# Optimization experiments

Hardware: AMD Instinct MI355X
Metric: run time of the kernel (lower is better)

The kernel has to match this reference:

```python
import jax, jax.numpy as jnp
import numpy as np

B, S, D = 1, 2048, 2048
NH, NKV, HD = 16, 8, 128
FF = 8192
L = 2
V = 32000
THETA = 10000.0
EPS = 1e-5
SCALE = 0.02


def setup_inputs() -> dict:
    key = jax.random.key(0)
    ks = jax.random.split(key, 16)
    return {
        "input_ids": jax.random.randint(ks[0], (B, S), 0, V, dtype=jnp.int32),
        "embed": jax.random.normal(ks[1], (V, D), jnp.float32) * SCALE,
        "Wq": jax.random.normal(ks[2], (L, D, NH * HD), jnp.float32) * SCALE,
        "Wk": jax.random.normal(ks[3], (L, D, NKV * HD), jnp.float32) * SCALE,
        "Wv": jax.random.normal(ks[4], (L, D, NKV * HD), jnp.float32) * SCALE,
        "Wo": jax.random.normal(ks[5], (L, NH * HD, D), jnp.float32) * SCALE,
        "Wgate": jax.random.normal(ks[6], (L, D, FF), jnp.float32) * SCALE,
        "Wup": jax.random.normal(ks[7], (L, D, FF), jnp.float32) * SCALE,
        "Wdown": jax.random.normal(ks[8], (L, FF, D), jnp.float32) * SCALE,
        "norm_attn": jnp.ones((L, D), jnp.float32),
        "norm_mlp": jnp.ones((L, D), jnp.float32),
        "norm_final": jnp.ones((D,), jnp.float32),
        "lm_head": jax.random.normal(ks[9], (D, V), jnp.float32) * SCALE,
        "D1": jax.random.normal(ks[10], (S,), jnp.float32) + 2.0,
        "D2": jax.random.normal(ks[11], (HD,), jnp.float32) + 2.0,
        "D3": jax.random.normal(ks[12], (S,), jnp.float32) + 2.0,
    }


def _rms_norm(x, w):
    return x * jax.lax.rsqrt(jnp.mean(x * x, axis=-1, keepdims=True) + EPS) * w


def _rotate_half(x):
    x1, x2 = jnp.split(x, 2, axis=-1)
    return jnp.concatenate([-x2, x1], axis=-1)


def _forward(input_ids, embed, Wq, Wk, Wv, Wo, Wgate, Wup, Wdown,
             norm_attn, norm_mlp, norm_final, lm_head, D1, D2, D3):
    # RoPE tables: [1,1,S,HD]
    inv_freq = 1.0 / (THETA ** (jnp.arange(0, HD, 2, dtype=jnp.float32) / HD))
    freqs = jnp.arange(S, dtype=jnp.float32)[:, None] * inv_freq[None, :]
    emb = jnp.concatenate([freqs, freqs], axis=-1)
    cos = jnp.cos(emb)[None, None]
    sin = jnp.sin(emb)[None, None]
    causal = jnp.tril(jnp.ones((S, S), dtype=bool))
    neg = jnp.finfo(jnp.float32).min
    D1i, D2i, D3i = 1.0 / D1, 1.0 / D2, 1.0 / D3
    n_rep = NH // NKV

    h = embed[input_ids]  # [B,S,D]
    for l in range(L):
        # --- attention block ---
        x = _rms_norm(h, norm_attn[l])
        q = (x @ Wq[l]).reshape(B, S, NH, HD).transpose(0, 2, 1, 3)   # [B,NH,S,HD]
        k = (x @ Wk[l]).reshape(B, S, NKV, HD).transpose(0, 2, 1, 3)  # [B,NKV,S,HD]
        v = (x @ Wv[l]).reshape(B, S, NKV, HD).transpose(0, 2, 1, 3)
        q = q * cos + _rotate_half(q) * sin
        k = k * cos + _rotate_half(k) * sin
        # repeat_kv (GQA)
        k = jnp.repeat(k, n_rep, axis=1)
        v = jnp.repeat(v, n_rep, axis=1)
        # TEE diagonal encryption: Q' = D1 Q D2, K'^T = D2^-1 K^T D3
        q_enc = q * D1[None, None, :, None] * D2[None, None, None, :]
        k_enc = k * D3[None, None, :, None] * D2i[None, None, None, :]
        scores = jnp.einsum('bhqd,bhkd->bhqk', q_enc, k_enc)
        # decrypt: D1^-1 (Q'K'^T) D3^-1  (mathematically cancels encryption)
        scores = scores * D1i[None, None, :, None] * D3i[None, None, None, :]
        scores = scores / jnp.sqrt(jnp.float32(HD))
        scores = jnp.where(causal[None, None], scores, neg)
        probs = jax.nn.softmax(scores, axis=-1)
        o = jnp.einsum('bhqk,bhkd->bhqd', probs, v)
        o = o.transpose(0, 2, 1, 3).reshape(B, S, NH * HD)
        h = h + o @ Wo[l]
        # --- SwiGLU MLP block ---
        x = _rms_norm(h, norm_mlp[l])
        h = h + (jax.nn.silu(x @ Wgate[l]) * (x @ Wup[l])) @ Wdown[l]

    h = _rms_norm(h, norm_final)
    return h @ lm_head  # logits [B,S,V]


def reference(input_ids, embed, Wq, Wk, Wv, Wo, Wgate, Wup, Wdown,
              norm_attn, norm_mlp, norm_final, lm_head, D1, D2, D3):
    return _forward(input_ids, embed, Wq, Wk, Wv, Wo, Wgate, Wup, Wdown,
                    norm_attn, norm_mlp, norm_final, lm_head, D1, D2, D3)
```

## Files before the change

### kernel.cpp

```cpp
#include <hip/hip_runtime.h>
#include <cstdint>
#include <cstddef>

typedef __attribute__((ext_vector_type(4))) float f32x4;
typedef __attribute__((ext_vector_type(8))) short short8;
typedef __attribute__((ext_vector_type(4))) unsigned int u32x4;

static const int TS = 2048;
static const int DM = 2048;
static const int NHEAD = 16, NKVH = 8, HDIM = 128;
static const int FFD = 8192;
static const int NVOC = 32000;
static const int QKVN = 4096;

__device__ __forceinline__ unsigned short f2bf(float f){
  unsigned int u = __builtin_bit_cast(unsigned int, f);
  u += 0x7FFFu + ((u >> 16) & 1u);
  return (unsigned short)(u >> 16);
}
__device__ __forceinline__ float bf2f(short h){
  unsigned int u = ((unsigned int)(unsigned short)h) << 16;
  return __builtin_bit_cast(float, u);
}
__device__ __forceinline__ f32x4 mfma16(short8 a, short8 b, f32x4 c){
  return __builtin_amdgcn_mfma_f32_16x16x32_bf16(a, b, c, 0, 0, 0);
}
__device__ __forceinline__ void gload16(const void* g, void* l){
  __builtin_amdgcn_global_load_lds(
      (const __attribute__((address_space(1))) unsigned int*)g,
      (__attribute__((address_space(3))) unsigned int*)l, 16, 0, 0);
}

__global__ void rope_tables_k(float* __restrict__ cosT, float* __restrict__ sinT){
  int idx = blockIdx.x * 256 + threadIdx.x;
  int s = idx >> 6, j = idx & 63;
  float inv = exp2f(-(float)j * (13.287712379549449f / 64.0f));
  float ang = (float)s * inv;
  cosT[idx] = cosf(ang);
  sinT[idx] = sinf(ang);
}

__global__ void embed_k(const int* __restrict__ ids, const float* __restrict__ E,
                        float* __restrict__ h){
  int s = blockIdx.x, tid = threadIdx.x;
  long id = ids[s];
  const f32x4* src = (const f32x4*)(E + id * (long)DM);
  f32x4* dst = (f32x4*)(h + (long)s * DM);
  dst[tid] = src[tid];
  dst[tid + 256] = src[tid + 256];
}

__global__ void rmsnorm_k(const float* __restrict__ x, const float* __restrict__ w,
                          short* __restrict__ out){
  int s = blockIdx.x, tid = threadIdx.x;
  const float* row = x + (long)s * DM;
  f32x4 v0 = *(const f32x4*)&row[tid * 8];
  f32x4 v1 = *(const f32x4*)&row[tid * 8 + 4];
  float ss = v0[0]*v0[0] + v0[1]*v0[1] + v0[2]*v0[2] + v0[3]*v0[3]
           + v1[0]*v1[0] + v1[1]*v1[1] + v1[2]*v1[2] + v1[3]*v1[3];
  #pragma unroll
  for (int off = 32; off; off >>= 1) ss += __shfl_xor(ss, off);
  __shared__ float sred[4];
  int wave = tid >> 6, lane = tid & 63;
  if (lane == 0) sred[wave] = ss;
  __syncthreads();
  float tot = sred[0] + sred[1] + sred[2] + sred[3];
  float r = rsqrtf(tot * (1.0f / (float)DM) + 1e-5f);
  f32x4 w0 = *(const f32x4*)&w[tid * 8];
  f32x4 w1 = *(const f32x4*)&w[tid * 8 + 4];
  short8 o;
  #pragma unroll
  for (int j = 0; j < 4; j++) o[j] = (short)f2bf(v0[j] * r * w0[j]);
  #pragma unroll
  for (int j = 0; j < 4; j++) o[4 + j] = (short)f2bf(v1[j] * r * w1[j]);
  *(short8*)&out[(long)s * DM + tid * 8] = o;
}

__global__ void transpose_k(const float* __restrict__ B, short* __restrict__ Bt,
                            int K, int N){
  __shared__ float t[64][65];
  int tid = threadIdx.x;
  int kb = blockIdx.y * 64, nb = blockIdx.x * 64;
  int r0 = tid >> 4, c4 = tid & 15;
  #pragma unroll
  for (int p = 0; p < 4; p++){
    int r = r0 + p * 16;
    f32x4 v = *(const f32x4*)&B[(long)(kb + r) * N + nb + c4 * 4];
    t[r][c4*4+0] = v[0]; t[r][c4*4+1] = v[1]; t[r][c4*4+2] = v[2]; t[r][c4*4+3] = v[3];
  }
  __syncthreads();
  int n0 = tid >> 3, k0 = (tid & 7) * 8;
  #pragma unroll
  for (int p = 0; p < 2; p++){
    int n = n0 + p * 32;
    short8 o;
    #pragma unroll
    for (int j = 0; j < 8; j++) o[j] = (short)f2bf(t[k0 + j][n]);
    *(short8*)&Bt[(long)(nb + n) * K + kb + k0] = o;
  }
}

__global__ void vtrans_k(const short* __restrict__ vb, short* __restrict__ vtb, int stride){
  int s0 = blockIdx.x * 64, kv = blockIdx.y;
  int tid = threadIdx.x;
  int s = s0 + (tid & 63);
  int d0 = (tid >> 6) * 8;
  #pragma unroll
  for (int p = 0; p < 4; p++){
    int d = d0 + p * 32;
    short8 v = *(const short8*)&vb[(long)s * stride + kv * HDIM + d];
    #pragma unroll
    for (int j = 0; j < 8; j++)
      vtb[(long)(kv * HDIM + d + j) * TS + s] = v[j];
  }
}

__global__ void rope_apply_k(short* __restrict__ buf, const float* __restrict__ cosT,
                             const float* __restrict__ sinT, int nh, int stride, int coloff){
  int idx = blockIdx.x * 256 + threadIdx.x;
  int j = idx & 63;
  int t = idx >> 6;
  int hh = t % nh;
  int s = t / nh;
  long base = (long)s * stride + coloff + hh * HDIM + j;
  float c = cosT[s * 64 + j], sn = sinT[s * 64 + j];
  float x1 = bf2f(buf[base]), x2 = bf2f(buf[base + 64]);
  buf[base]      = (short)f2bf(x1 * c - x2 * sn);
  buf[base + 64] = (short)f2bf(x2 * c + x1 * sn);
}

__global__ void reduce4_k(const float* __restrict__ p, float* __restrict__ h){
  const long stride = (long)TS * DM;
  long i = ((long)blockIdx.x * 256 + threadIdx.x) * 4;
  f32x4 a = *(const f32x4*)&h[i];
  f32x4 v0 = *(const f32x4*)&p[i];
  f32x4 v1 = *(const f32x4*)&p[i + stride];
  f32x4 v2 = *(const f32x4*)&p[i + 2 * stride];
  f32x4 v3 = *(const f32x4*)&p[i + 3 * stride];
  a = a + ((v0 + v1) + (v2 + v3));
  *(f32x4*)&h[i] = a;
}

template<int EPI>
__global__ __launch_bounds__(512, 2)
void gemm256(const short* __restrict__ A, int lda,
             const short* __restrict__ Bt, int ldb,
             float* __restrict__ Cf, short* __restrict__ Cb,
             const short* __restrict__ Xtra, int N, int K){
  __shared__ short lds[2][2][16384];
  const int tid = threadIdx.x;
  const int wid = tid >> 6, lane = tid & 63;
  const int wr = wid >> 2, wc = wid & 3;
  const int fr = lane & 15, fch = lane >> 4;
  const int nt = K >> 6;
  const int nIter = nt >> 1;

  const int z = blockIdx.y;
  A  += (long)z * K;
  Bt += (long)z * K;

  const int nbt = N >> 8;
  const int nwg = nbt << 3;
  const int q = nwg >> 3;
  const int swz = (blockIdx.x & 7) * q + (blockIdx.x >> 3);
  const int mb = swz & 7, nb = swz >> 3;

  const short* Abase = A  + (long)(mb * 256 + fr) * lda + fch * 8;
  const short* Bbase = Bt + (long)(nb * 256 + fr) * ldb + fch * 8;
  const int gA = ((wid >> 2) << 3) | (wid & 3);
  const int gB = ((wid >> 1) << 2) | (wid & 1);

  short8 a[4][2], b[2][2];
  f32x4 acc[8][4] = {};

#define STAGE_A(buf, beta, tau) do{ \
    const int g_ = gA | ((beta) << 2); \
    const short* gp_ = Abase + (long)(g_ * 16) * lda + (long)(tau) * 64; \
    gload16(gp_,      &lds[buf][0][(g_ * 2 + 0) * 512]); \
    gload16(gp_ + 32, &lds[buf][0][(g_ * 2 + 1) * 512]); \
  }while(0)
#define STAGE_B(buf, beta, tau) do{ \
    const int g_ = gB | ((beta) << 1); \
    const short* gp_ = Bbase + (long)(g_ * 16) * ldb + (long)(tau) * 64; \
    gload16(gp_,      &lds[buf][1][(g_ * 2 + 0) * 512]); \
    gload16(gp_ + 32, &lds[buf][1][(g_ * 2 + 1) * 512]); \
  }while(0)
#define LDA(buf, mh) do{ \
    _Pragma("unroll") \
    for (int j_ = 0; j_ < 4; j_++){ \
      const int o_ = (wr * 8 + (mh) * 4 + j_) * 1024 + fch * 128 + fr * 8; \
      a[j_][0] = *(const short8*)&lds[buf][0][o_]; \
      a[j_][1] = *(const short8*)&lds[buf][0][o_ + 512]; \
    } }while(0)
#define LDB(buf, nh) do{ \
    _Pragma("unroll") \
    for (int j_ = 0; j_ < 2; j_++){ \
      const int o_ = (wc * 4 + (nh) * 2 + j_) * 1024 + fch * 128 + fr * 8; \
      b[j_][0] = *(const short8*)&lds[buf][1][o_]; \
      b[j_][1] = *(const short8*)&lds[buf][1][o_ + 512]; \
    } }while(0)
#define SYNC_MF(mh, nh) do{ \
    __builtin_amdgcn_s_barrier(); \
    asm volatile("s_waitcnt lgkmcnt(0)" ::: "memory"); \
    __builtin_amdgcn_s_setprio(1); \
    _Pragma("unroll") \
    for (int j_ = 0; j_ < 4; j_++) \
      _Pragma("unroll") \
      for (int i_ = 0; i_ < 2; i_++){ \
        acc[(mh)*4+j_][(nh)*2+i_] = mfma16(a[j_][0], b[i_][0], acc[(mh)*4+j_][(nh)*2+i_]); \
        acc[(mh)*4+j_][(nh)*2+i_] = mfma16(a[j_][1], b[i_][1], acc[(mh)*4+j_][(nh)*2+i_]); \
      } \
    __builtin_amdgcn_s_setprio(0); \
    __builtin_amdgcn_s_barrier(); \
  }while(0)

  STAGE_A(0, 0, 0); STAGE_B(0, 0, 0); STAGE_B(0, 1, 0); STAGE_A(0, 1, 0);
  STAGE_A(1, 0, 1); STAGE_B(1, 1, 1); STAGE_A(1, 1, 1);
  asm volatile("s_waitcnt vmcnt(6)" ::: "memory");
  __builtin_amdgcn_s_barrier();

  for (int it = 0; it < nIter; ++it){
    const int t = it * 2;
    const int t2 = (t + 2 < nt) ? t + 2 : nt - 1;
    const int t3 = (t + 3 < nt) ? t + 3 : nt - 1;
    LDA(0, 0); LDB(0, 0); STAGE_B(1, 0, t + 1);
    SYNC_MF(0, 0);
    LDB(0, 1); STAGE_A(0, 0, t2);
    SYNC_MF(0, 1);
    LDA(0, 1); STAGE_B(0, 1, t2);
    SYNC_MF(1, 1);
    LDB(0, 0); STAGE_A(0, 1, t2);
    asm volatile("s_waitcnt vmcnt(6)" ::: "memory");
    SYNC_MF(1, 0);
    LDA(1, 0); LDB(1, 0); STAGE_B(0, 0, t2);
    SYNC_MF(0, 0);
    LDB(1, 1); STAGE_A(1, 0, t3);
    SYNC_MF(0, 1);
    LDA(1, 1); STAGE_B(1, 1, t3);
    SYNC_MF(1, 1);
    LDB(1, 0); STAGE_A(1, 1, t3);
    asm volatile("s_waitcnt vmcnt(6)" ::: "memory");
    SYNC_MF(1, 0);
  }
  asm volatile("s_waitcnt vmcnt(0)" ::: "memory");

#undef STAGE_A
#undef STAGE_B
#undef LDA
#undef LDB
#undef SYNC_MF

  const int rb0 = mb * 256 + wr * 128 + fch * 4;
  const int cb0 = nb * 256 + wc * 64 + fr;
  const long pbase = (EPI == 5) ? (long)z * ((long)TS * N) : 0;
  #pragma unroll
  for (int m = 0; m < 8; m++)
    #pragma unroll
    for (int n = 0; n < 4; n++)
      #pragma unroll
      for (int i = 0; i < 4; i++){
        long idx = (long)(rb0 + m * 16 + i) * N + (cb0 + n * 16);
        float v = acc[m][n][i];
        if constexpr (EPI == 0) Cf[idx] = v;
        else if constexpr (EPI == 1) Cb[idx] = (short)f2bf(v);
        else if constexpr (EPI == 3){
          float sg = 1.0f / (1.0f + __expf(-v));
          Cb[idx] = (short)f2bf(v * sg);
        } else if constexpr (EPI == 4){
          float g = bf2f(Xtra[idx]);
          Cb[idx] = (short)f2bf(g * v);
        } else {
          Cf[pbase + idx] = v;
        }
      }
}

template<int EPI>
__global__ __launch_bounds__(256)
void gemm_bt(const short* __restrict__ A, const short* __restrict__ Bt,
             float* __restrict__ Cf, short* __restrict__ Cb,
             const short* __restrict__ Xtra, int N, int K){
  __shared__ short As[4096];
  __shared__ short Bs[4096];
  const int tid = threadIdx.x;
  const int wave = tid >> 6, lane = tid & 63;
  const int wr = wave >> 1, wc = wave & 1;
  const int mb = blockIdx.y, nb = blockIdx.x;

  const int srow = lane & 15;
  const int scol = (lane >> 4) * 8;
  const short* ApL0 = A + (long)(mb * 128 + wave * 16 + srow) * K + scol;
  const short* ApL1 = ApL0 + (long)64 * K;
  const short* BpL0 = Bt + (long)(nb * 128 + wave * 16 + srow) * K + scol;
  const short* BpL1 = BpL0 + (long)64 * K;

  f32x4 acc[4][4] = {};
  const int fr = lane & 15, fch = lane >> 4;

  for (int kb = 0; kb < K; kb += 32){
    __syncthreads();
    gload16(ApL0 + kb, &As[wave * 512]);
    gload16(ApL1 + kb, &As[(4 + wave) * 512]);
    gload16(BpL0 + kb, &Bs[wave * 512]);
    gload16(BpL1 + kb, &Bs[(4 + wave) * 512]);
    __syncthreads();
    short8 a[4], b[4];
    #pragma unroll
    for (int m = 0; m < 4; m++)
      a[m] = *(const short8*)&As[(wr * 4 + m) * 512 + fch * 128 + fr * 8];
    #pragma unroll
    for (int n = 0; n < 4; n++)
      b[n] = *(const short8*)&Bs[(wc * 4 + n) * 512 + fch * 128 + fr * 8];
    #pragma unroll
    for (int m = 0; m < 4; m++)
      #pragma unroll
      for (int n = 0; n < 4; n++)
        acc[m][n] = mfma16(a[m], b[n], acc[m][n]);
  }

  const int rb = mb * 128 + wr * 64 + (lane >> 4) * 4;
  const int cb = nb * 128 + wc * 64 + (lane & 15);
  #pragma unroll
  for (int m = 0; m < 4; m++)
    #pragma unroll
    for (int n = 0; n < 4; n++)
      #pragma unroll
      for (int i = 0; i < 4; i++){
        long idx = (long)(rb + m * 16 + i) * N + (cb + n * 16);
        float v = acc[m][n][i];
        if constexpr (EPI == 0) Cf[idx] = v;
        else if constexpr (EPI == 1) Cb[idx] = (short)f2bf(v);
        else if constexpr (EPI == 2) Cf[idx] += v;
        else if constexpr (EPI == 3){
          float sg = 1.0f / (1.0f + __expf(-v));
          Cb[idx] = (short)f2bf(v * sg);
        } else {
          float g = bf2f(Xtra[idx]);
          Cb[idx] = (short)f2bf(g * v);
        }
      }
}

__device__ __forceinline__ int qoff(int r, int cB){ return r * 256 + (cB ^ ((r & 7) << 4)); }
__device__ __forceinline__ int voff(int d, int cB){ return d * 128 + (cB ^ ((d & 7) << 4)); }
__device__ __forceinline__ int poff(int r, int cB){ return r * 128 + (cB ^ ((r & 7) << 4)); }

__global__ __launch_bounds__(256)
void attn_k(const short* __restrict__ qb, const short* __restrict__ kb,
            const short* __restrict__ vtb, short* __restrict__ ob){
  __shared__ short Qs[64 * 128];
  __shared__ short Ks[64 * 128];
  __shared__ short Vt[128 * 64];
  __shared__ short Ps[64 * 64];
  const int tid = threadIdx.x, wave = tid >> 6, lane = tid & 63;
  const int qt = blockIdx.x, head = blockIdx.y, kvh = head >> 1;
  const float scale = 0.08838834764831845f;

  {
    int r0 = tid >> 4, c16 = tid & 15;
    #pragma unroll
    for (int p = 0; p < 4; p++){
      int r = r0 + p * 16;
      u32x4 v = *(const u32x4*)&qb[(long)(qt * 64 + r) * QKVN + head * HDIM + c16 * 8];
      *(u32x4*)((char*)Qs + qoff(r, c16 * 16)) = v;
    }
  }

  float mrun[4] = {-1e30f, -1e30f, -1e30f, -1e30f};
  float lrun[4] = {0.f, 0.f, 0.f, 0.f};
  f32x4 accO[8] = {};

  for (int kt = 0; kt <= qt; kt++){
    __syncthreads();
    {
      int r0 = tid >> 4, c16 = tid & 15;
      #pragma unroll
      for (int p = 0; p < 4; p++){
        int r = r0 + p * 16;
        u32x4 v = *(const u32x4*)&kb[(long)(kt * 64 + r) * QKVN + kvh * HDIM + c16 * 8];
        *(u32x4*)((char*)Ks + qoff(r, c16 * 16)) = v;
      }
      int vr0 = tid >> 3, vc = tid & 7;
      #pragma unroll
      for (int p = 0; p < 4; p++){
        int d = vr0 + p * 32;
        u32x4 v = *(const u32x4*)&vtb[(long)(kvh * HDIM + d) * TS + kt * 64 + vc * 8];
        *(u32x4*)((char*)Vt + voff(d, vc * 16)) = v;
      }
    }
    __syncthreads();

    f32x4 sacc[4] = {};
    #pragma unroll
    for (int k4 = 0; k4 < 4; k4++){
      short8 aq = *(const short8*)((const char*)Qs +
                   qoff(wave * 16 + (lane & 15), k4 * 64 + (lane >> 4) * 16));
      #pragma unroll
      for (int n = 0; n < 4; n++){
        short8 bk = *(const short8*)((const char*)Ks +
                     qoff(n * 16 + (lane & 15), k4 * 64 + (lane >> 4) * 16));
        sacc[n] = mfma16(aq, bk, sacc[n]);
      }
    }

    const bool diag = (kt == qt);
    float mt[4] = {-1e30f, -1e30f, -1e30f, -1e30f};
    #pragma unroll
    for (int n = 0; n < 4; n++)
      #pragma unroll
      for (int i = 0; i < 4; i++){
        float v = sacc[n][i] * scale;
        if (diag){
          int rr = (lane >> 4) * 4 + i + wave * 16;
          int cc = n * 16 + (lane & 15);
          if (cc > rr) v = -1e30f;
        }
        sacc[n][i] = v;
        mt[i] = fmaxf(mt[i], v);
      }
    #pragma unroll
    for (int off = 1; off < 16; off <<= 1)
      #pragma unroll
      for (int i = 0; i < 4; i++) mt[i] = fmaxf(mt[i], __shfl_xor(mt[i], off));
    float alpha[4], rsum[4];
    #pragma unroll
    for (int i = 0; i < 4; i++){
      float mn = fmaxf(mrun[i], mt[i]);
      alpha[i] = __expf(mrun[i] - mn);
      mrun[i] = mn;
      rsum[i] = 0.f;
    }
    #pragma unroll
    for (int n = 0; n < 4; n++)
      #pragma unroll
      for (int i = 0; i < 4; i++){
        float p = __expf(sacc[n][i] - mrun[i]);
        sacc[n][i] = p;
        rsum[i] += p;
      }
    #pragma unroll
    for (int off = 1; off < 16; off <<= 1)
      #pragma unroll
      for (int i = 0; i < 4; i++) rsum[i] += __shfl_xor(rsum[i], off);
    #pragma unroll
    for (int i = 0; i < 4; i++) lrun[i] = lrun[i] * alpha[i] + rsum[i];

    #pragma unroll
    for (int n = 0; n < 4; n++)
      #pragma unroll
      for (int i = 0; i < 4; i++){
        int rr = wave * 16 + (lane >> 4) * 4 + i;
        int cc = n * 16 + (lane & 15);
        *(short*)((char*)Ps + poff(rr, cc * 2)) = (short)f2bf(sacc[n][i]);
      }

    #pragma unroll
    for (int n = 0; n < 8; n++)
      #pragma unroll
      for (int i = 0; i < 4; i++) accO[n][i] *= alpha[i];
    #pragma unroll
    for (int ks = 0; ks < 2; ks++){
      short8 ap = *(const short8*)((const char*)Ps +
                   poff(wave * 16 + (lane & 15), ks * 64 + (lane >> 4) * 16));
      #pragma unroll
      for (int n = 0; n < 8; n++){
        short8 bv = *(const short8*)((const char*)Vt +
                     voff(n * 16 + (lane & 15), ks * 64 + (lane >> 4) * 16));
        accO[n] = mfma16(ap, bv, accO[n]);
      }
    }
  }

  #pragma unroll
  for (int i = 0; i < 4; i++){
    float inv = 1.0f / lrun[i];
    int rr = qt * 64 + wave * 16 + (lane >> 4) * 4 + i;
    #pragma unroll
    for (int n = 0; n < 8; n++){
      int cc = head * HDIM + n * 16 + (lane & 15);
      ob[(long)rr * DM + cc] = (short)f2bf(accO[n][i] * inv);
    }
  }
}

extern "C" void kernel_launch(void* const* d_in, const int* in_sizes, int n_in,
                              void* d_out, int out_size, void* d_ws, size_t ws_size,
                              hipStream_t stream){
  (void)in_sizes; (void)n_in; (void)out_size; (void)ws_size;
  const int*   ids = (const int*)d_in[0];
  const float* E   = (const float*)d_in[1];
  const float* Wq  = (const float*)d_in[2];
  const float* Wk  = (const float*)d_in[3];
  const float* Wv  = (const float*)d_in[4];
  const float* Wo  = (const float*)d_in[5];
  const float* Wg  = (const float*)d_in[6];
  const float* Wu  = (const float*)d_in[7];
  const float* Wd  = (const float*)d_in[8];
  const float* nA  = (const float*)d_in[9];
  const float* nM  = (const float*)d_in[10];
  const float* nF  = (const float*)d_in[11];
  const float* LMH = (const float*)d_in[12];
  float* out = (float*)d_out;

  char* ws = (char*)d_ws;
  size_t off = 0;
  auto alloc = [&](size_t bytes){ void* p = ws + off; off += (bytes + 255) & ~(size_t)255; return p; };
  float* h    = (float*)alloc((size_t)TS * DM * 4);
  short* xb   = (short*)alloc((size_t)TS * DM * 2);
  short* qkvb = (short*)alloc((size_t)TS * QKVN * 2);
  short* vtb  = (short*)alloc((size_t)NKVH * HDIM * TS * 2);
  short* obuf = (short*)alloc((size_t)TS * DM * 2);
  short* sg   = (short*)alloc((size_t)TS * FFD * 2);
  short* actb = (short*)alloc((size_t)TS * FFD * 2);
  float* cosT = (float*)alloc((size_t)TS * 64 * 4);
  float* sinT = (float*)alloc((size_t)TS * 64 * 4);
  short* wT   = (short*)alloc((size_t)NVOC * DM * 2);
  float* pPart = (float*)((char*)wT + (size_t)36 * 1024 * 1024);

  rope_tables_k<<<512, 256, 0, stream>>>(cosT, sinT);
  embed_k<<<TS, 256, 0, stream>>>(ids, E, h);

  for (int l = 0; l < 2; l++){
    rmsnorm_k<<<TS, 256, 0, stream>>>(h, nA + (size_t)l * DM, xb);
    transpose_k<<<dim3(32, 32), 256, 0, stream>>>(Wq + (size_t)l * DM * DM, wT, DM, DM);
    transpose_k<<<dim3(16, 32), 256, 0, stream>>>(Wk + (size_t)l * DM * 1024, wT + (size_t)2048 * DM, DM, 1024);
    transpose_k<<<dim3(16, 32), 256, 0, stream>>>(Wv + (size_t)l * DM * 1024, wT + (size_t)3072 * DM, DM, 1024);
    gemm256<1><<<dim3(128), 512, 0, stream>>>(xb, DM, wT, DM, nullptr, qkvb, nullptr, QKVN, DM);
    rope_apply_k<<<8192, 256, 0, stream>>>(qkvb, cosT, sinT, NHEAD, QKVN, 0);
    rope_apply_k<<<4096, 256, 0, stream>>>(qkvb, cosT, sinT, NKVH, QKVN, 2048);
    vtrans_k<<<dim3(32, 8), 256, 0, stream>>>(qkvb + 3072, vtb, QKVN);
    attn_k<<<dim3(32, 16), 256, 0, stream>>>(qkvb, qkvb + 2048, vtb, obuf);
    transpose_k<<<dim3(32, 32), 256, 0, stream>>>(Wo + (size_t)l * DM * DM, wT, DM, DM);
    gemm_bt<2><<<dim3(16, 16), 256, 0, stream>>>(obuf, wT, h, nullptr, nullptr, DM, DM);
    rmsnorm_k<<<TS, 256, 0, stream>>>(h, nM + (size_t)l * DM, xb);
    transpose_k<<<dim3(128, 32), 256, 0, stream>>>(Wg + (size_t)l * DM * FFD, wT, DM, FFD);
    gemm256<3><<<dim3(256), 512, 0, stream>>>(xb, DM, wT, DM, nullptr, sg, nullptr, FFD, DM);
    transpose_k<<<dim3(128, 32), 256, 0, stream>>>(Wu + (size_t)l * DM * FFD, wT, DM, FFD);
    gemm256<4><<<dim3(256), 512, 0, stream>>>(xb, DM, wT, DM, nullptr, actb, sg, FFD, DM);
    transpose_k<<<dim3(32, 128), 256, 0, stream>>>(Wd + (size_t)l * FFD * DM, wT, FFD, DM);
    gemm256<5><<<dim3(64, 4), 512, 0, stream>>>(actb, FFD, wT, FFD, pPart, nullptr, nullptr, DM, FFD / 4);
    reduce4_k<<<4096, 256, 0, stream>>>(pPart, h);
  }

  rmsnorm_k<<<TS, 256, 0, stream>>>(h, nF, xb);
  transpose_k<<<dim3(500, 32), 256, 0, stream>>>(LMH, wT, DM, NVOC);
  gemm256<0><<<dim3(1000), 512, 0, stream>>>(xb, DM, wT, DM, out, nullptr, nullptr, NVOC, DM);
}
```

Baseline: 1.543 ms.

## Restructure GEMM mainloop to 4-buffer K=32 pipeline with register ping-pong

Rewrites the gemm256 main loop so each K step is 32 wide instead of 64, and rotates four LDS buffers instead of two. Fragments are held in even/odd register sets so the next tile's LDS reads overlap the current MFMAs. This cuts barriers per MFMA group, from two per 8-MFMA block to two per tile, and uses sched_barrier to keep loads interleaved with compute. The risks are a deeper prefetch with tighter vmcnt accounting and shorter K tiles, which mean more iterations and more loop overhead. The final vmcnt(0) drain was also removed.

```diff
diff --git a/kernel.cpp b/kernel.cpp
--- a/kernel.cpp
+++ b/kernel.cpp
@@ -147,13 +147,12 @@
              const short* __restrict__ Bt, int ldb,
              float* __restrict__ Cf, short* __restrict__ Cb,
              const short* __restrict__ Xtra, int N, int K){
-  __shared__ short lds[2][2][16384];
+  __shared__ short lds[4][2][8192];
   const int tid = threadIdx.x;
   const int wid = tid >> 6, lane = tid & 63;
   const int wr = wid >> 2, wc = wid & 3;
   const int fr = lane & 15, fch = lane >> 4;
-  const int nt = K >> 6;
-  const int nIter = nt >> 1;
+  const int nt = K >> 5;
 
   const int z = blockIdx.y;
   A  += (long)z * K;
@@ -167,88 +166,69 @@
 
   const short* Abase = A  + (long)(mb * 256 + fr) * lda + fch * 8;
   const short* Bbase = Bt + (long)(nb * 256 + fr) * ldb + fch * 8;
-  const int gA = ((wid >> 2) << 3) | (wid & 3);
-  const int gB = ((wid >> 1) << 2) | (wid & 1);
-
-  short8 a[4][2], b[2][2];
+  const int gA0 = wid * 2, gA1 = wid * 2 + 1;
+
+  short8 aE[4], aO[4], bE[2], bO[2];
   f32x4 acc[8][4] = {};
 
-#define STAGE_A(buf, beta, tau) do{ \
-    const int g_ = gA | ((beta) << 2); \
-    const short* gp_ = Abase + (long)(g_ * 16) * lda + (long)(tau) * 64; \
-    gload16(gp_,      &lds[buf][0][(g_ * 2 + 0) * 512]); \
-    gload16(gp_ + 32, &lds[buf][0][(g_ * 2 + 1) * 512]); \
+#define STG_A(bufc, g_, tau_) \
+  gload16(Abase + (long)((g_) * 16) * lda + (long)(tau_) * 32, &lds[bufc][0][(g_) * 512])
+#define STG_B(bufc, g_, tau_) \
+  gload16(Bbase + (long)((g_) * 16) * ldb + (long)(tau_) * 32, &lds[bufc][1][(g_) * 512])
+#define RDA(dst, bufc, mh) do{ \
+    _Pragma("unroll") \
+    for (int j_ = 0; j_ < 4; j_++) \
+      dst[j_] = *(const short8*)&lds[bufc][0][(wr * 8 + (mh) * 4 + j_) * 512 + fch * 128 + fr * 8]; \
   }while(0)
-#define STAGE_B(buf, beta, tau) do{ \
-    const int g_ = gB | ((beta) << 1); \
-    const short* gp_ = Bbase + (long)(g_ * 16) * ldb + (long)(tau) * 64; \
-    gload16(gp_,      &lds[buf][1][(g_ * 2 + 0) * 512]); \
-    gload16(gp_ + 32, &lds[buf][1][(g_ * 2 + 1) * 512]); \
+#define RDB(dst, bufc, nh) do{ \
+    _Pragma("unroll") \
+    for (int i_ = 0; i_ < 2; i_++) \
+      dst[i_] = *(const short8*)&lds[bufc][1][(wc * 4 + (nh) * 2 + i_) * 512 + fch * 128 + fr * 8]; \
   }while(0)
-#define LDA(buf, mh) do{ \
-    _Pragma("unroll") \
-    for (int j_ = 0; j_ < 4; j_++){ \
-      const int o_ = (wr * 8 + (mh) * 4 + j_) * 1024 + fch * 128 + fr * 8; \
-      a[j_][0] = *(const short8*)&lds[buf][0][o_]; \
-      a[j_][1] = *(const short8*)&lds[buf][0][o_ + 512]; \
-    } }while(0)
-#define LDB(buf, nh) do{ \
-    _Pragma("unroll") \
-    for (int j_ = 0; j_ < 2; j_++){ \
-      const int o_ = (wc * 4 + (nh) * 2 + j_) * 1024 + fch * 128 + fr * 8; \
-      b[j_][0] = *(const short8*)&lds[buf][1][o_]; \
-      b[j_][1] = *(const short8*)&lds[buf][1][o_ + 512]; \
-    } }while(0)
-#define SYNC_MF(mh, nh) do{ \
-    __builtin_amdgcn_s_barrier(); \
-    asm volatile("s_waitcnt lgkmcnt(0)" ::: "memory"); \
+#define MM8(va, vb, mh, nh) do{ \
     __builtin_amdgcn_s_setprio(1); \
     _Pragma("unroll") \
     for (int j_ = 0; j_ < 4; j_++) \
       _Pragma("unroll") \
-      for (int i_ = 0; i_ < 2; i_++){ \
-        acc[(mh)*4+j_][(nh)*2+i_] = mfma16(a[j_][0], b[i_][0], acc[(mh)*4+j_][(nh)*2+i_]); \
-        acc[(mh)*4+j_][(nh)*2+i_] = mfma16(a[j_][1], b[i_][1], acc[(mh)*4+j_][(nh)*2+i_]); \
-      } \
+      for (int i_ = 0; i_ < 2; i_++) \
+        acc[(mh)*4+j_][(nh)*2+i_] = mfma16(va[j_], vb[i_], acc[(mh)*4+j_][(nh)*2+i_]); \
     __builtin_amdgcn_s_setprio(0); \
+  }while(0)
+#define SB __builtin_amdgcn_sched_barrier(0)
+
+#define TILE(t_, bufR, bufN, bufS, bC, bNx) do{ \
+    const int tau_ = ((t_) + 2 < nt) ? (t_) + 2 : nt - 1; \
+    RDB(bNx, bufR, 1); STG_A(bufS, gA0, tau_); SB; MM8(aE, bC, 0, 0); \
+    RDA(aO,  bufR, 1); STG_A(bufS, gA1, tau_); SB; MM8(aE, bNx, 0, 1); \
+    asm volatile("s_waitcnt vmcnt(2)" ::: "memory"); \
+    __builtin_amdgcn_s_barrier(); \
+    RDA(aE,  bufN, 0); STG_B(bufS, gA0, tau_); SB; MM8(aO, bNx, 1, 1); \
+    RDB(bNx, bufN, 0); STG_B(bufS, gA1, tau_); SB; MM8(aO, bC, 1, 0); \
     __builtin_amdgcn_s_barrier(); \
   }while(0)
 
-  STAGE_A(0, 0, 0); STAGE_B(0, 0, 0); STAGE_B(0, 1, 0); STAGE_A(0, 1, 0);
-  STAGE_A(1, 0, 1); STAGE_B(1, 1, 1); STAGE_A(1, 1, 1);
-  asm volatile("s_waitcnt vmcnt(6)" ::: "memory");
+  STG_A(0, gA0, 0); STG_A(0, gA1, 0); STG_B(0, gA0, 0); STG_B(0, gA1, 0);
+  STG_A(1, gA0, 1); STG_A(1, gA1, 1); STG_B(1, gA0, 1); STG_B(1, gA1, 1);
+  asm volatile("s_waitcnt vmcnt(4)" ::: "memory");
   __builtin_amdgcn_s_barrier();
-
+  RDA(aE, 0, 0); RDB(bE, 0, 0);
+
+  const int nIter = nt >> 2;
   for (int it = 0; it < nIter; ++it){
-    const int t = it * 2;
-    const int t2 = (t + 2 < nt) ? t + 2 : nt - 1;
-    const int t3 = (t + 3 < nt) ? t + 3 : nt - 1;
-    LDA(0, 0); LDB(0, 0); STAGE_B(1, 0, t + 1);
-    SYNC_MF(0, 0);
-    LDB(0, 1); STAGE_A(0, 0, t2);
-    SYNC_MF(0, 1);
-    LDA(0, 1); STAGE_B(0, 1, t2);
-    SYNC_MF(1, 1);
-    LDB(0, 0); STAGE_A(0, 1, t2);
-    asm volatile("s_waitcnt vmcnt(6)" ::: "memory");
-    SYNC_MF(1, 0);
-    LDA(1, 0); LDB(1, 0); STAGE_B(0, 0, t2);
-    SYNC_MF(0, 0);
-    LDB(1, 1); STAGE_A(1, 0, t3);
-    SYNC_MF(0, 1);
-    LDA(1, 1); STAGE_B(1, 1, t3);
-    SYNC_MF(1, 1);
-    LDB(1, 0); STAGE_A(1, 1, t3);
-    asm volatile("s_waitcnt vmcnt(6)" ::: "memory");
-    SYNC_MF(1, 0);
-  }
-  asm volatile("s_waitcnt vmcnt(0)" ::: "memory");
-
-#undef STAGE_A
-#undef STAGE_B
-#undef LDA
-#undef LDB
-#undef SYNC_MF
+    const int t0 = it << 2;
+    TILE(t0 + 0, 0, 1, 2, bE, bO);
+    TILE(t0 + 1, 1, 2, 3, bO, bE);
+    TILE(t0 + 2, 2, 3, 0, bE, bO);
+    TILE(t0 + 3, 3, 0, 1, bO, bE);
+  }
+
+#undef STG_A
+#undef STG_B
+#undef RDA
+#undef RDB
+#undef MM8
+#undef SB
+#undef TILE
 
   const int rb0 = mb * 256 + wr * 128 + fch * 4;
   const int cb0 = nb * 256 + wc * 64 + fr;
```

New measurement: 1.546 ms. Within noise of the previous version (+0.2%).
